# Performance work log

Hardware: AMD Instinct MI355X
Metric: run time of the kernel (lower is better)

Reference implementation:

```python
import jax, jax.numpy as jnp
import numpy as np

S = 610      # number of HMM states (~6*nCodons+10 for nCodons=100)
E = 126      # order-transformed emission alphabet
BATCH = 32
T = 2048
NREG = 5000  # number of punished transitions
ALPHA_REG = 4.0


def setup_inputs() -> dict:
    key = jax.random.key(0)
    k1, k2, k3, k4, k5, k6 = jax.random.split(key, 6)
    obs = jax.random.randint(k1, (BATCH, T), 0, E)
    inputs = jax.nn.one_hot(obs, E, dtype=jnp.float32)          # [B,T,E]
    A = jax.nn.softmax(jax.random.normal(k2, (S, S)), axis=-1)   # row-stochastic transitions
    Bm = jax.nn.softmax(jax.random.normal(k3, (S, E)), axis=-1)  # emission matrix
    I = jax.nn.softmax(jax.random.normal(k4, (S,)))              # initial distribution
    reg_from = jax.random.randint(k5, (NREG,), 0, S)
    reg_to = jax.random.randint(k6, (NREG,), 0, S)
    return {"inputs": inputs, "A": A, "Bm": Bm, "I": I,
            "reg_from": reg_from, "reg_to": reg_to}


def reference(inputs, A, Bm, I, reg_from, reg_to):
    # emission likelihoods per step: [B,T,S]
    em = jnp.einsum('bte,se->bts', inputs, Bm)

    # HMM forward recursion with per-step normalization (scaled forward algorithm)
    alpha0 = I[None, :] * em[:, 0]                # [B,S]
    z0 = alpha0.sum(-1, keepdims=True)
    carry0 = (alpha0 / z0, jnp.log(z0[:, 0]))

    def step(carry, em_t):
        alpha, ll = carry
        a = (alpha @ A) * em_t                    # [B,S]
        z = a.sum(-1, keepdims=True)
        return (a / z, ll + jnp.log(z[:, 0])), None

    em_tbs = jnp.swapaxes(em, 0, 1)               # [T,B,S]
    (alpha_T, loglik), _ = jax.lax.scan(step, carry0, em_tbs[1:])

    loglik_mean = jnp.mean(loglik)
    # regularization: mean of log(1 - A[f, t]) over punished transitions
    reg_mean = jnp.mean(jnp.log1p(-A[reg_from, reg_to]))
    loss = -loglik_mean - ALPHA_REG * reg_mean
    return loss
```

## Files before the change

### kernel.cpp

```cpp
#include <hip/hip_runtime.h>
#include <math.h>

#define S      610
#define E      126
#define BATCH  32
#define T      2048
#define NREG   5000

#define SPAD   640
#define NT     40
#define NCH    5
#define MBXG   4
#define NBLK   8
#define THREADS 512
#define NWAVE  8
#define TPW    5
#define RT     3
#define AROW   672

typedef float f32x4 __attribute__((ext_vector_type(4)));
typedef int   i32x8 __attribute__((ext_vector_type(8)));

union Frag { uint4 q[2]; i32x8 v; };

#define MFMA_SCALED(af, bf, acc) \
    __builtin_amdgcn_mfma_scale_f32_16x16x128_f8f6f4((af), (bf), (acc), 0, 0, \
                                                     0, 0x7F7F7F7F, 0, 0x7F7F7F7F)

__device__ __forceinline__ float fastrcp(float x) {
#if __has_builtin(__builtin_amdgcn_rcpf)
    return __builtin_amdgcn_rcpf(x);
#else
    return 1.f / x;
#endif
}

__device__ __forceinline__ void ldsbar() {
#if __has_builtin(__builtin_amdgcn_s_waitcnt) && __has_builtin(__builtin_amdgcn_s_barrier)
    __builtin_amdgcn_s_waitcnt(0xC07F);
    __builtin_amdgcn_s_barrier();
#else
    __syncthreads();
#endif
}

template <int CTRL>
__device__ __forceinline__ float rotf(float v) {
    int r = __builtin_amdgcn_update_dpp(0, __builtin_bit_cast(int, v),
                                        CTRL, 0xF, 0xF, true);
    return __builtin_bit_cast(float, r);
}
__device__ __forceinline__ float row16_sum(float v) {
    v += rotf<0x128>(v);
    v += rotf<0x124>(v);
    v += rotf<0x122>(v);
    v += rotf<0x121>(v);
    return v;
}

__device__ __host__ __forceinline__ int posf(int j) {
    int n = j >> 4, mr = j & 15;
    return (n < 32) ? ((n & 7) * 16 + mr) * 4 + (n >> 3)
                    : 512 + (n - 32) * 16 + mr;
}
__device__ __forceinline__ int inv_pos(int p) {
    if (p < 512) {
        int idx = p & 3, q = p >> 2;
        return (idx * 8 + (q >> 4)) * 16 + (q & 15);
    }
    int q = p - 512;
    return (32 + (q >> 4)) * 16 + (q & 15);
}

__device__ __forceinline__ unsigned sw_e4m3_enc(float f) {
    if (!(f > 0.f)) return 0u;
    int e; float fr = frexpf(f, &e);
    if (e - 1 < -6) {
        int q = (int)rintf(f * 512.f);
        if (q > 7) q = 7;
        return (unsigned)q;
    }
    int m = (int)rintf(fr * 16.f) - 8;
    int EE = e - 1;
    if (m == 8) { m = 0; EE += 1; }
    if (EE > 8) { EE = 8; m = 7; }
    return (unsigned)(((EE + 7) << 3) | m);
}
__device__ __forceinline__ unsigned pack_quad(float v0, float v1, float v2, float v3) {
#if __has_builtin(__builtin_amdgcn_cvt_pk_fp8_f32)
    int w = 0;
    w = __builtin_amdgcn_cvt_pk_fp8_f32(v0, v1, w, false);
    w = __builtin_amdgcn_cvt_pk_fp8_f32(v2, v3, w, true);
    return (unsigned)w;
#else
    return sw_e4m3_enc(v0) | (sw_e4m3_enc(v1) << 8) |
           (sw_e4m3_enc(v2) << 16) | (sw_e4m3_enc(v3) << 24);
#endif
}
__device__ __forceinline__ unsigned char fp8byte(float v) {
#if __has_builtin(__builtin_amdgcn_cvt_pk_fp8_f32)
    int w = __builtin_amdgcn_cvt_pk_fp8_f32(v, v, 0, false);
    return (unsigned char)(w & 0xFF);
#else
    return (unsigned char)sw_e4m3_enc(v);
#endif
}

__global__ void k_init(unsigned* __restrict__ maxbuf) { maxbuf[0] = 0u; }

__global__ void k_max(const float* __restrict__ A, unsigned* __restrict__ maxbuf) {
    int tid = blockIdx.x * blockDim.x + threadIdx.x;
    float m = 0.f;
    for (int i = tid; i < S * S; i += gridDim.x * blockDim.x) m = fmaxf(m, A[i]);
#pragma unroll
    for (int off = 1; off < 64; off <<= 1) m = fmaxf(m, __shfl_xor(m, off, 64));
    if ((threadIdx.x & 63) == 0) atomicMax(maxbuf, __float_as_uint(m));
}

__global__ void k_scalefin(const unsigned* __restrict__ maxbuf,
                           float* __restrict__ s_out, double* __restrict__ logs_out) {
    float mx = __uint_as_float(maxbuf[0]);
    float s = 224.f / mx;
    s_out[0] = s;
    logs_out[0] = log((double)s);
}

__global__ void k_pack8mx(const float* __restrict__ A, const float* __restrict__ s_in,
                          uint4* __restrict__ A8c) {
    int n = blockIdx.x;
    int c = blockIdx.y;
    int l = threadIdx.x;
    float s = s_in[0];
    int j = n * 16 + (l & 15);
    int pb0 = c * 128 + (l >> 4) * 32;
#pragma unroll
    for (int h = 0; h < 2; ++h) {
        unsigned dw[4];
#pragma unroll
        for (int r = 0; r < 4; ++r) {
            float v[4];
#pragma unroll
            for (int pb = 0; pb < 4; ++pb) {
                int k = inv_pos(pb0 + h * 16 + r * 4 + pb);
                v[pb] = (k < S && j < S) ? A[k * S + j] * s : 0.f;
            }
            dw[r] = pack_quad(v[0], v[1], v[2], v[3]);
        }
        A8c[((n * NCH + c) * 2 + h) * 64 + l] = make_uint4(dw[0], dw[1], dw[2], dw[3]);
    }
}

__global__ void k_bmt(const float* __restrict__ Bm, float* __restrict__ BmT) {
    int j = threadIdx.x;
    int o = blockIdx.x;
    BmT[o * SPAD + j] = (j < S) ? Bm[j * E + o] : 0.f;
}

__global__ void k_obs(const float* __restrict__ in, int* __restrict__ obsT) {
    int i = blockIdx.x * blockDim.x + threadIdx.x;
    if (i >= BATCH * T) return;
    const float2* p = (const float2*)(in + (size_t)i * E);
    int o = 0;
#pragma unroll
    for (int k = 0; k < E / 2; ++k) {
        float2 v = p[k];
        if (v.x > 0.5f) o = 2 * k;
        if (v.y > 0.5f) o = 2 * k + 1;
    }
    int b = i / T, t = i % T;
    obsT[t * BATCH + b] = o * SPAD;
}

__global__ void k_reg(const float* __restrict__ A, const int* __restrict__ rf,
                      const int* __restrict__ rt, float* __restrict__ out) {
    __shared__ float wpart[16];
    int tid = threadIdx.x;
    float s = 0.f;
    for (int i = tid; i < NREG; i += 1024)
        s += log1pf(-A[rf[i] * S + rt[i]]);
#pragma unroll
    for (int off = 1; off < 64; off <<= 1) s += __shfl_xor(s, off, 64);
    if ((tid & 63) == 0) wpart[tid >> 6] = s;
    __syncthreads();
    if (tid == 0) {
        float t = 0.f;
        for (int w = 0; w < 16; ++w) t += wpart[w];
        out[0] = t;
    }
}

__global__ __launch_bounds__(THREADS, 2) void k_forward(
    const uint4* __restrict__ A8c,
    const float* __restrict__ BmT,
    const int*   __restrict__ obsT,
    const float* __restrict__ Iv,
    const double* __restrict__ logs,
    double* __restrict__ ll_out)
{
    __shared__ __align__(16) uint4 pinAv[8 * NCH * 2 * 64];
    __shared__ __align__(16) unsigned char alphaq[MBXG * AROW];
    __shared__ __align__(16) float zpart[NWAVE][MBXG];
    __shared__ __align__(64) float zT[MBXG][8];
    __shared__ __align__(16) float zsc[MBXG];
    __shared__ __align__(16) float zf[MBXG];

    const int g    = blockIdx.x;
    const int tid  = threadIdx.x;
    const int wv   = tid >> 6;
    const int lane = tid & 63;
    const int mrow = lane & 15;
    const int quad = lane >> 4;
    const int b0   = g * MBXG;

    for (int i = tid; i < 8 * NCH * 2 * 64; i += THREADS)
        pinAv[i] = A8c[24 * NCH * 2 * 64 + i];

    i32x8 areg[RT][NCH];
#pragma unroll
    for (int rt = 0; rt < RT; ++rt)
#pragma unroll
        for (int c = 0; c < NCH; ++c) {
            Frag f;
            f.q[0] = A8c[(((rt * 8 + wv) * NCH + c) * 2 + 0) * 64 + lane];
            f.q[1] = A8c[(((rt * 8 + wv) * NCH + c) * 2 + 1) * 64 + lane];
            areg[rt][c] = f.v;
        }

    double ll = 0.0;
    {
        const int j1 = tid + THREADS;
        const bool hasb = (j1 < SPAD);
        float Ia = (tid < S) ? Iv[tid] : 0.f;
        float Ib = (hasb && j1 < S) ? Iv[j1] : 0.f;
        float v0a[MBXG], v0b[MBXG], p0[MBXG];
#pragma unroll
        for (int m = 0; m < MBXG; ++m) {
            int o = obsT[b0 + m];
            v0a[m] = Ia * BmT[o + tid];
            v0b[m] = hasb ? Ib * BmT[o + j1] : 0.f;
            p0[m] = v0a[m] + v0b[m];
        }
#pragma unroll
        for (int off = 1; off < 64; off <<= 1)
#pragma unroll
            for (int m = 0; m < MBXG; ++m) p0[m] += __shfl_xor(p0[m], off, 64);
        if (lane == 0) {
#pragma unroll
            for (int m = 0; m < MBXG; ++m) zpart[wv][m] = p0[m];
        }
        __syncthreads();
        if (tid < MBXG) {
            float z = 0.f;
            for (int w = 0; w < NWAVE; ++w) z += zpart[w][tid];
            zf[tid]  = z;
            zsc[tid] = 128.f / z;
        }
        __syncthreads();
        const int pa = posf(tid);
        const int pb = hasb ? posf(j1) : 0;
#pragma unroll
        for (int m = 0; m < MBXG; ++m) {
            alphaq[m * AROW + pa] = fp8byte(v0a[m] * zsc[m]);
            if (hasb) alphaq[m * AROW + pb] = fp8byte(v0b[m] * zsc[m]);
        }
        __syncthreads();
        if (wv == 0) ll = (double)__logf(zf[quad]);
    }

    const uint4* sp   = A8c + (size_t)((32 + wv) * NCH * 2) * 64 + lane;
    const uint4* pinp = pinAv + wv * (NCH * 2 * 64) + lane;
    const unsigned char* aqp = alphaq + (mrow >> 2) * AROW + quad * 32;

    int jrow[TPW];
#pragma unroll
    for (int idx = 0; idx < TPW; ++idx) {
        const int n = (idx < 4) ? (idx * 8 + wv) : (32 + wv);
        jrow[idx] = n * 16 + mrow;
    }

    float em[TPW];
    {
        const int o = obsT[1 * BATCH + b0 + quad];
#pragma unroll
        for (int idx = 0; idx < TPW; ++idx) em[idx] = BmT[o + jrow[idx]];
    }

    i32x8 gs[3];
    {
        Frag f; f.q[0] = sp[0];   f.q[1] = sp[64];  gs[0] = f.v;
    }
    {
        Frag f; f.q[0] = sp[128]; f.q[1] = sp[192]; gs[1] = f.v;
    }

    float zprev = 1.f;

    for (int t = 1; t < T; ++t) {
        i32x8 afc[2], pfc[2];
        {
            Frag f; f.q[0] = *(const uint4*)(aqp); f.q[1] = *(const uint4*)(aqp + 16);
            afc[0] = f.v;
        }
        {
            Frag f; f.q[0] = pinp[0]; f.q[1] = pinp[64]; pfc[0] = f.v;
        }

        f32x4 acc[TPW];
#pragma unroll
        for (int idx = 0; idx < TPW; ++idx) acc[idx] = (f32x4)0.f;

#pragma unroll
        for (int c = 0; c < NCH; ++c) {
            if (c + 2 < NCH) {
                Frag f;
                f.q[0] = sp[((c + 2) * 2 + 0) * 64];
                f.q[1] = sp[((c + 2) * 2 + 1) * 64];
                gs[(c + 2) % 3] = f.v;
            }
            if (c + 1 < NCH) {
                Frag f;
                f.q[0] = *(const uint4*)(aqp + (c + 1) * 128);
                f.q[1] = *(const uint4*)(aqp + (c + 1) * 128 + 16);
                afc[(c + 1) & 1] = f.v;
                Frag p;
                p.q[0] = pinp[(c + 1) * 128];
                p.q[1] = pinp[(c + 1) * 128 + 64];
                pfc[(c + 1) & 1] = p.v;
            }
            const i32x8 a = afc[c & 1];
#pragma unroll
            for (int rt = 0; rt < RT; ++rt)
                acc[rt] = MFMA_SCALED(a, areg[rt][c], acc[rt]);
            acc[3] = MFMA_SCALED(a, pfc[c & 1], acc[3]);
            acc[4] = MFMA_SCALED(a, gs[c % 3], acc[4]);
        }

        if (wv == 0) ll += (double)__logf(zprev);

        const int tn = (t + 1 < T) ? t + 1 : t;
        const int on = obsT[tn * BATCH + b0 + quad];

        float pz = 0.f;
#pragma unroll
        for (int idx = 0; idx < TPW; ++idx) {
            em[idx] = acc[idx][0] * em[idx];
            pz += em[idx];
        }
        pz = row16_sum(pz);
        if (mrow == 0) zT[quad][wv] = pz;
        ldsbar();

        const f32x4 za = *(const f32x4*)(&zT[quad][0]);
        const f32x4 zb = *(const f32x4*)(&zT[quad][4]);
        const f32x4 s4 = za + zb;
        const float z  = (s4[0] + s4[1]) + (s4[2] + s4[3]);
        const float iv = 128.f * fastrcp(z);
        zprev = z;

        {
            const int wbase = (wv * 16 + mrow) * 4;
            unsigned dw = pack_quad(em[0] * iv, em[1] * iv, em[2] * iv, em[3] * iv);
            *(unsigned*)(alphaq + quad * AROW + wbase) = dw;
            alphaq[quad * AROW + 512 + wv * 16 + mrow] = fp8byte(em[4] * iv);
        }
#pragma unroll
        for (int idx = 0; idx < TPW; ++idx) em[idx] = BmT[on + jrow[idx]];
        {
            Frag f; f.q[0] = sp[0];   f.q[1] = sp[64];  gs[0] = f.v;
        }
        {
            Frag f; f.q[0] = sp[128]; f.q[1] = sp[192]; gs[1] = f.v;
        }
        ldsbar();
    }

    if (wv == 0) ll += (double)__logf(zprev);

    const double LOG128 = 4.852030263919617;
    if (wv == 0 && mrow == 0)
        ll_out[b0 + quad] = ll - 2047.0 * (logs[0] + LOG128);
}

__global__ void k_final(const double* __restrict__ ll, const float* __restrict__ regsum,
                        float* __restrict__ out) {
    double s = 0.0;
    for (int b = 0; b < BATCH; ++b) s += ll[b];
    double loglik_mean = s / BATCH;
    double reg_mean = (double)regsum[0] / NREG;
    out[0] = (float)(-loglik_mean - 4.0 * reg_mean);
}

extern "C" void kernel_launch(void* const* d_in, const int* in_sizes, int n_in,
                              void* d_out, int out_size, void* d_ws, size_t ws_size,
                              hipStream_t stream) {
    const float* inputs = (const float*)d_in[0];
    const float* A      = (const float*)d_in[1];
    const float* Bm     = (const float*)d_in[2];
    const float* Iv     = (const float*)d_in[3];
    const int*   rf     = (const int*)d_in[4];
    const int*   rt     = (const int*)d_in[5];

    char* ws = (char*)d_ws;
    uint4*    A8c  = (uint4*)ws;
    float*    BmT  = (float*)(ws + 409600);
    int*      obsT = (int*)(ws + 732160);
    double*   ll   = (double*)(ws + 994304);
    float*    regs = (float*)(ws + 994560);
    unsigned* mx   = (unsigned*)(ws + 994564);
    float*    sbuf = (float*)(ws + 994568);
    double*   logs = (double*)(ws + 994576);

    hipLaunchKernelGGL(k_init,     dim3(1),   dim3(1),   0, stream, mx);
    hipLaunchKernelGGL(k_max,      dim3(256), dim3(256), 0, stream, A, mx);
    hipLaunchKernelGGL(k_scalefin, dim3(1),   dim3(1),   0, stream, mx, sbuf, logs);
    hipLaunchKernelGGL(k_pack8mx,  dim3(NT, NCH), dim3(64), 0, stream, A, sbuf, A8c);
    hipLaunchKernelGGL(k_bmt,      dim3(E),   dim3(SPAD), 0, stream, Bm, BmT);
    hipLaunchKernelGGL(k_obs,      dim3((BATCH * T + 255) / 256), dim3(256), 0, stream, inputs, obsT);
    hipLaunchKernelGGL(k_reg,      dim3(1),   dim3(1024), 0, stream, A, rf, rt, regs);
    hipLaunchKernelGGL(k_forward,  dim3(NBLK), dim3(THREADS), 0, stream,
                       A8c, BmT, obsT, Iv, logs, ll);
    hipLaunchKernelGGL(k_final,    dim3(1),   dim3(1),   0, stream, ll, regs, (float*)d_out);
}
```

Before: 2.532 ms.

## Double-buffer alpha and defer normalization to remove one barrier per step

The forward loop now double-buffers the quantized alpha and partial-sum arrays in LDS. Each step normalizes with the previous step's sum, rescaled by the average A scale over E, instead of waiting for the current step's sum. This drops one of the two block barriers per time step on the serial recurrence. The log-likelihood is rebuilt from the accumulated scale factors plus a final-sum term. This trades exact per-step normalization for an approximate scale, which risks fp8 range drift if the estimate is poor.

New measurement: 2.297 ms. 1.1x faster.

```diff
diff --git a/kernel.cpp b/kernel.cpp
--- a/kernel.cpp
+++ b/kernel.cpp
@@ -17,6 +17,7 @@
 #define TPW    5
 #define RT     3
 #define AROW   672
+#define ABUF   (MBXG * AROW)
 
 typedef float f32x4 __attribute__((ext_vector_type(4)));
 typedef int   i32x8 __attribute__((ext_vector_type(8)));
@@ -122,6 +123,7 @@
     float mx = __uint_as_float(maxbuf[0]);
     float s = 224.f / mx;
     s_out[0] = s;
+    s_out[1] = s / (float)E;
     logs_out[0] = log((double)s);
 }
 
@@ -194,15 +196,15 @@
     const float* __restrict__ BmT,
     const int*   __restrict__ obsT,
     const float* __restrict__ Iv,
+    const float* __restrict__ sbuf,
     const double* __restrict__ logs,
     double* __restrict__ ll_out)
 {
     __shared__ __align__(16) uint4 pinAv[8 * NCH * 2 * 64];
-    __shared__ __align__(16) unsigned char alphaq[MBXG * AROW];
+    __shared__ __align__(16) unsigned char alphaq[2 * ABUF];
     __shared__ __align__(16) float zpart[NWAVE][MBXG];
-    __shared__ __align__(64) float zT[MBXG][8];
+    __shared__ __align__(64) float zT[2][MBXG][8];
     __shared__ __align__(16) float zsc[MBXG];
-    __shared__ __align__(16) float zf[MBXG];
 
     const int g    = blockIdx.x;
     const int tid  = threadIdx.x;
@@ -212,6 +214,8 @@
     const int quad = lane >> 4;
     const int b0   = g * MBXG;
 
+    const float rhobar = sbuf[1];
+
     for (int i = tid; i < 8 * NCH * 2 * 64; i += THREADS)
         pinAv[i] = A8c[24 * NCH * 2 * 64 + i];
 
@@ -226,7 +230,7 @@
             areg[rt][c] = f.v;
         }
 
-    double ll = 0.0;
+    double gls = 0.0;
     {
         const int j1 = tid + THREADS;
         const bool hasb = (j1 < SPAD);
@@ -249,10 +253,10 @@
             for (int m = 0; m < MBXG; ++m) zpart[wv][m] = p0[m];
         }
         __syncthreads();
+        if (tid < 32) zT[0][tid & 3][tid >> 2] = zpart[tid >> 2][tid & 3];
         if (tid < MBXG) {
             float z = 0.f;
             for (int w = 0; w < NWAVE; ++w) z += zpart[w][tid];
-            zf[tid]  = z;
             zsc[tid] = 128.f / z;
         }
         __syncthreads();
@@ -264,12 +268,12 @@
             if (hasb) alphaq[m * AROW + pb] = fp8byte(v0b[m] * zsc[m]);
         }
         __syncthreads();
-        if (wv == 0) ll = (double)__logf(zf[quad]);
-    }
+    }
+    float iv_prev = zsc[quad];
 
     const uint4* sp   = A8c + (size_t)((32 + wv) * NCH * 2) * 64 + lane;
     const uint4* pinp = pinAv + wv * (NCH * 2 * 64) + lane;
-    const unsigned char* aqp = alphaq + (mrow >> 2) * AROW + quad * 32;
+    const int aoff = (mrow >> 2) * AROW + quad * 32;
 
     int jrow[TPW];
 #pragma unroll
@@ -293,9 +297,11 @@
         Frag f; f.q[0] = sp[128]; f.q[1] = sp[192]; gs[1] = f.v;
     }
 
-    float zprev = 1.f;
-
     for (int t = 1; t < T; ++t) {
+        const int rb = (t - 1) & 1;
+        const unsigned char* aqp = alphaq + rb * ABUF + aoff;
+        unsigned char*       aqw = alphaq + (rb ^ 1) * ABUF;
+
         i32x8 afc[2], pfc[2];
         {
             Frag f; f.q[0] = *(const uint4*)(aqp); f.q[1] = *(const uint4*)(aqp + 16);
@@ -335,7 +341,14 @@
             acc[4] = MFMA_SCALED(a, gs[c % 3], acc[4]);
         }
 
-        if (wv == 0) ll += (double)__logf(zprev);
+        const f32x4 za = *(const f32x4*)(&zT[rb][quad][0]);
+        const f32x4 zb = *(const f32x4*)(&zT[rb][quad][4]);
+        const f32x4 s4 = za + zb;
+        const float zpm  = (s4[0] + s4[1]) + (s4[2] + s4[3]);
+        const float zd   = fmaxf(zpm * iv_prev * rhobar, 1e-30f);
+        const float ivq  = 128.f * fastrcp(zd);
+        if (wv == 0) gls += (double)__logf(iv_prev);
+        iv_prev = ivq;
 
         const int tn = (t + 1 < T) ? t + 1 : t;
         const int on = obsT[tn * BATCH + b0 + quad];
@@ -346,23 +359,15 @@
             em[idx] = acc[idx][0] * em[idx];
             pz += em[idx];
         }
-        pz = row16_sum(pz);
-        if (mrow == 0) zT[quad][wv] = pz;
-        ldsbar();
-
-        const f32x4 za = *(const f32x4*)(&zT[quad][0]);
-        const f32x4 zb = *(const f32x4*)(&zT[quad][4]);
-        const f32x4 s4 = za + zb;
-        const float z  = (s4[0] + s4[1]) + (s4[2] + s4[3]);
-        const float iv = 128.f * fastrcp(z);
-        zprev = z;
-
         {
             const int wbase = (wv * 16 + mrow) * 4;
-            unsigned dw = pack_quad(em[0] * iv, em[1] * iv, em[2] * iv, em[3] * iv);
-            *(unsigned*)(alphaq + quad * AROW + wbase) = dw;
-            alphaq[quad * AROW + 512 + wv * 16 + mrow] = fp8byte(em[4] * iv);
-        }
+            unsigned dw = pack_quad(em[0] * ivq, em[1] * ivq, em[2] * ivq, em[3] * ivq);
+            *(unsigned*)(aqw + quad * AROW + wbase) = dw;
+            aqw[quad * AROW + 512 + wv * 16 + mrow] = fp8byte(em[4] * ivq);
+        }
+        pz = row16_sum(pz);
+        if (mrow == 0) zT[rb ^ 1][quad][wv] = pz;
+
 #pragma unroll
         for (int idx = 0; idx < TPW; ++idx) em[idx] = BmT[on + jrow[idx]];
         {
@@ -374,11 +379,15 @@
         ldsbar();
     }
 
-    if (wv == 0) ll += (double)__logf(zprev);
-
-    const double LOG128 = 4.852030263919617;
-    if (wv == 0 && mrow == 0)
-        ll_out[b0 + quad] = ll - 2047.0 * (logs[0] + LOG128);
+    {
+        const int fb = (T - 1) & 1;
+        const f32x4 za = *(const f32x4*)(&zT[fb][quad][0]);
+        const f32x4 zb = *(const f32x4*)(&zT[fb][quad][4]);
+        const f32x4 s4 = za + zb;
+        const float zfin = (s4[0] + s4[1]) + (s4[2] + s4[3]);
+        if (wv == 0 && mrow == 0)
+            ll_out[b0 + quad] = (double)__logf(zfin) - gls - 2047.0 * logs[0];
+    }
 }
 
 __global__ void k_final(const double* __restrict__ ll, const float* __restrict__ regsum,
@@ -418,6 +427,6 @@
     hipLaunchKernelGGL(k_obs,      dim3((BATCH * T + 255) / 256), dim3(256), 0, stream, inputs, obsT);
     hipLaunchKernelGGL(k_reg,      dim3(1),   dim3(1024), 0, stream, A, rf, rt, regs);
     hipLaunchKernelGGL(k_forward,  dim3(NBLK), dim3(THREADS), 0, stream,
-                       A8c, BmT, obsT, Iv, logs, ll);
+                       A8c, BmT, obsT, Iv, sbuf, logs, ll);
     hipLaunchKernelGGL(k_final,    dim3(1),   dim3(1),   0, stream, ll, regs, (float*)d_out);
 }
```
